# Optimization experiments

Measured on AMD Instinct MI355X. Metric: run time of the kernel, lower is better.

Reference implementation:

```python
import jax, jax.numpy as jnp
import numpy as np

B, T, D = 1, 2048, 4096
H, G = 32, 8
HD = D // H          # 128
REP = H // G         # 4
KV_DIM = 2 * HD * G  # 2048


def setup_inputs() -> dict:
    key = jax.random.key(0)
    k0, k1, k2, k3 = jax.random.split(key, 4)
    x = jax.random.normal(k0, (B, T, D), dtype=jnp.float32)
    Wq = jax.random.normal(k1, (D, D), dtype=jnp.float32) * 0.02
    Wkv = jax.random.normal(k2, (D, KV_DIM), dtype=jnp.float32) * 0.02
    Wo = jax.random.normal(k3, (D, D), dtype=jnp.float32) * 0.02
    bo = jnp.zeros((D,), dtype=jnp.float32)
    return {"x": x, "Wq": Wq, "Wkv": Wkv, "Wo": Wo, "bo": bo}


def reference(x, Wq, Wkv, Wo, bo):
    b, t, d = x.shape
    # projections (qkv_bias=False)
    q = jnp.dot(x, Wq).reshape(b, t, H, HD).transpose(0, 2, 1, 3)        # (b,H,t,hd)
    kv = jnp.dot(x, Wkv).reshape(b, t, G, 2, HD).transpose(2, 3, 0, 1, 4)  # (G,2,b,t,hd)
    k, v = kv[:, 0], kv[:, 1]                                             # (G,b,t,hd)
    # faithful to torch: unsqueeze+repeat then flat view(b, H, t, hd)
    k = jnp.broadcast_to(k[:, :, None], (G, b, REP, t, HD)).reshape(b, H, t, HD)
    v = jnp.broadcast_to(v[:, :, None], (G, b, REP, t, HD)).reshape(b, H, t, HD)
    # attention: mask then scale, matching original order
    scores = jnp.einsum('bhqd,bhkd->bhqk', q, k)                          # (b,H,t,t)
    causal = jnp.triu(jnp.ones((t, t), dtype=bool), 1)
    scores = jnp.where(causal[None, None], -jnp.inf, scores)
    weights = jax.nn.softmax(scores * (1.0 / HD ** 0.5), axis=-1)
    ctx = jnp.einsum('bhqk,bhkd->bhqd', weights, v)                       # (b,H,t,hd)
    ctx = ctx.transpose(0, 2, 1, 3).reshape(b, t, d)
    return jnp.dot(ctx, Wo) + bo
```

## Files before the change

kernel.cpp:

```cpp
#include <hip/hip_runtime.h>

#define T_SEQ 2048
#define D_MODEL 4096
#define NH 32
#define NG 8
#define HD 128

typedef unsigned short u16;
typedef __bf16 bf16x8 __attribute__((ext_vector_type(8)));
typedef float f32x4 __attribute__((ext_vector_type(4)));

#define AS1 __attribute__((address_space(1)))
#define AS3 __attribute__((address_space(3)))

__device__ __forceinline__ void async_cp16(const u16* g, u16* l) {
  __builtin_amdgcn_global_load_lds((AS1 void*)g, (AS3 void*)l, 16, 0, 0);
}

__device__ __forceinline__ u16 f2bf(float f){
  union { float f; unsigned x; } v; v.f = f;
  unsigned r = v.x + 0x7FFFu + ((v.x >> 16) & 1u);
  return (u16)(r >> 16);
}
__device__ __forceinline__ u16 to_bf(float f){ return f2bf(f); }
__device__ __forceinline__ u16 to_bf(u16 u){ return u; }

__global__ __launch_bounds__(256) void cvt_k(const float* __restrict__ in,
                                             u16* __restrict__ out, int n4)
{
  int i = blockIdx.x * 256 + threadIdx.x;
  if (i >= n4) return;
  float4 v = *(const float4*)&in[(size_t)i * 4];
  short4 o;
  o.x = (short)f2bf(v.x); o.y = (short)f2bf(v.y);
  o.z = (short)f2bf(v.z); o.w = (short)f2bf(v.w);
  *(short4*)&out[(size_t)i * 4] = o;
}

template<typename TIN>
__global__ __launch_bounds__(256) void transpose_k(const TIN* __restrict__ in,
                                                   u16* __restrict__ out, int R, int C)
{
  __shared__ __align__(16) u16 tile[32][36];
  int c0 = blockIdx.x * 32, r0 = blockIdx.y * 32;
  int t = threadIdx.x;
  int lr = t >> 3, lc = (t & 7) * 4;
  const TIN* src = &in[(size_t)(r0 + lr) * C + c0 + lc];
  #pragma unroll
  for (int i = 0; i < 4; i++) tile[lr][lc + i] = to_bf(src[i]);
  __syncthreads();
  short4 v;
  v.x = (short)tile[lc + 0][lr];
  v.y = (short)tile[lc + 1][lr];
  v.z = (short)tile[lc + 2][lr];
  v.w = (short)tile[lc + 3][lr];
  *(short4*)&out[(size_t)(c0 + lr) * R + r0 + lc] = v;
}

template<int MODE>
__global__ __launch_bounds__(256) void gemm_k(
    const u16* __restrict__ A, const u16* __restrict__ BT,
    u16* __restrict__ Cout, u16* __restrict__ Kout, u16* __restrict__ Vout,
    float* __restrict__ Fout, const float* __restrict__ bias, int K, int N)
{
  __shared__ __align__(16) u16 sA[2 * 128 * 64];
  __shared__ __align__(16) u16 sB[2 * 128 * 64];
  const int t = threadIdx.x;
  const int lane = t & 63, wave = t >> 6;
  const int quad = lane >> 4, lm = lane & 15;
  const int wm = wave >> 1, wn = wave & 1;
  const int m0 = blockIdx.y * 128, n0 = blockIdx.x * 128;
  const int ntk = K >> 6;
  const f32x4 fzero = {0.f, 0.f, 0.f, 0.f};

  const int sr_sub = lane >> 3;
  const int sgl = (lane & 7) ^ sr_sub;

  f32x4 acc[4][4];
  #pragma unroll
  for (int i = 0; i < 4; i++)
    #pragma unroll
    for (int j = 0; j < 4; j++) acc[i][j] = fzero;

  auto stage = [&](int td) {
    const int k0 = td << 6;
    u16* dA = sA + (td & 1) * (128 * 64);
    u16* dB = sB + (td & 1) * (128 * 64);
    #pragma unroll
    for (int c = 0; c < 4; c++) {
      int r = c * 32 + wave * 8 + sr_sub;
      async_cp16(&A [(size_t)(m0 + r) * K + k0 + sgl * 8], &dA[(c * 256 + wave * 64) * 8]);
      async_cp16(&BT[(size_t)(n0 + r) * K + k0 + sgl * 8], &dB[(c * 256 + wave * 64) * 8]);
    }
  };

  stage(0);
  stage(1);

  for (int ti = 0; ti < ntk; ++ti) {
    if (ti + 1 < ntk) { asm volatile("s_waitcnt vmcnt(8)" ::: "memory"); }
    else             { asm volatile("s_waitcnt vmcnt(0)" ::: "memory"); }
    __builtin_amdgcn_s_barrier();
    asm volatile("" ::: "memory");

    const u16* cA = sA + (ti & 1) * (128 * 64);
    const u16* cB = sB + (ti & 1) * (128 * 64);

    __builtin_amdgcn_s_setprio(1);
    #pragma unroll
    for (int kb = 0; kb < 2; kb++) {
      bf16x8 af[4], bfr[4];
      #pragma unroll
      for (int mt = 0; mt < 4; mt++) {
        int row = wm * 64 + mt * 16 + lm;
        af[mt] = *(const bf16x8*)&cA[row * 64 + (((kb * 4 + quad) ^ (lm & 7)) * 8)];
      }
      #pragma unroll
      for (int nt = 0; nt < 4; nt++) {
        int row = wn * 64 + nt * 16 + lm;
        bfr[nt] = *(const bf16x8*)&cB[row * 64 + (((kb * 4 + quad) ^ (lm & 7)) * 8)];
      }
      #pragma unroll
      for (int mt = 0; mt < 4; mt++)
        #pragma unroll
        for (int nt = 0; nt < 4; nt++)
          acc[mt][nt] = __builtin_amdgcn_mfma_f32_16x16x32_bf16(af[mt], bfr[nt], acc[mt][nt], 0, 0, 0);
    }
    __builtin_amdgcn_s_setprio(0);

    __builtin_amdgcn_s_barrier();
    asm volatile("" ::: "memory");
    if (ti + 2 < ntk) stage(ti + 2);
  }

  #pragma unroll
  for (int mt = 0; mt < 4; mt++) {
    #pragma unroll
    for (int nt = 0; nt < 4; nt++) {
      int gcol = n0 + wn * 64 + nt * 16 + lm;
      int grow0 = m0 + wm * 64 + mt * 16 + quad * 4;
      if (MODE == 1) {
        if (gcol < 4096) {
          #pragma unroll
          for (int r = 0; r < 4; r++)
            Cout[(size_t)(grow0 + r) * 4096 + gcol] = f2bf(acc[mt][nt][r]);
        } else {
          int c = gcol - 4096;
          int g = c >> 8, s = (c >> 7) & 1, hd = c & 127;
          if (s) {
            short4 pv;
            pv.x = (short)f2bf(acc[mt][nt][0]);
            pv.y = (short)f2bf(acc[mt][nt][1]);
            pv.z = (short)f2bf(acc[mt][nt][2]);
            pv.w = (short)f2bf(acc[mt][nt][3]);
            *(short4*)&Vout[((size_t)g * HD + hd) * T_SEQ + grow0] = pv;
          } else {
            #pragma unroll
            for (int r = 0; r < 4; r++)
              Kout[((size_t)g * T_SEQ + grow0 + r) * HD + hd] = f2bf(acc[mt][nt][r]);
          }
        }
      } else {
        #pragma unroll
        for (int r = 0; r < 4; r++)
          Fout[(size_t)(grow0 + r) * N + gcol] = acc[mt][nt][r] + bias[gcol];
      }
    }
  }
}

__global__ __launch_bounds__(256) void attn_k(
    const u16* __restrict__ Q, const u16* __restrict__ Kb,
    const u16* __restrict__ Vt, u16* __restrict__ ctx)
{
  __shared__ __align__(16) u16 sK[2 * 64 * 128];
  __shared__ __align__(16) u16 sV[2 * 128 * 64];
  __shared__ __align__(16) u16 sP[4 * 16 * 72];
  const int t = threadIdx.x;
  const int lane = t & 63, wave = t >> 6;
  const int quad = lane >> 4, lm = lane & 15;

  const int id = blockIdx.x + gridDim.x * blockIdx.y;
  const int g = id & 7;
  const int idx = id >> 3;
  const int h = g * 4 + (idx & 3);
  const int q0 = (31 - (idx >> 2)) * 64;
  const int nt = (q0 >> 6) + 1;

  const float scale = 0.088388347648318447f;
  const float C1 = scale * 1.4426950408889634f;
  const float C2 = -14.0f * 1.4426950408889634f;
  const f32x4 fzero = {0.f, 0.f, 0.f, 0.f};

  bf16x8 aq[4];
  {
    const u16* qp = Q + (size_t)(q0 + wave * 16 + lm) * D_MODEL + h * HD + quad * 8;
    #pragma unroll
    for (int kb = 0; kb < 4; kb++) aq[kb] = *(const bf16x8*)(qp + kb * 32);
  }
  bf16x8 bones;
  #pragma unroll
  for (int i = 0; i < 8; i++) bones[i] = (__bf16)1.0f;

  f32x4 o[8];
  #pragma unroll
  for (int i = 0; i < 8; i++) o[i] = fzero;
  f32x4 lacc = fzero;

  const u16* Kg = Kb + (size_t)g * T_SEQ * HD;
  const u16* Vg = Vt + (size_t)g * HD * T_SEQ;
  u16* sPw = sP + wave * 16 * 72;

  const int k_r_sub = lane >> 4;
  const int v_r_sub = lane >> 3;
  const int v_gl = (lane & 7) ^ v_r_sub;

  auto stage = [&](int td) {
    const int kv0 = td << 6;
    u16* dK = sK + (td & 1) * (64 * 128);
    u16* dV = sV + (td & 1) * (128 * 64);
    #pragma unroll
    for (int c = 0; c < 4; c++) {
      int rk = c * 16 + wave * 4 + k_r_sub;
      int kgl = (lane & 15) ^ (rk & 7);
      async_cp16(&Kg[(size_t)(kv0 + rk) * HD + kgl * 8], &dK[(c * 256 + wave * 64) * 8]);
      int rv = c * 32 + wave * 8 + v_r_sub;
      async_cp16(&Vg[(size_t)rv * T_SEQ + kv0 + v_gl * 8], &dV[(c * 256 + wave * 64) * 8]);
    }
  };

  stage(0);
  if (nt > 1) stage(1);

  for (int ti = 0; ti < nt; ++ti) {
    if (ti + 1 < nt) { asm volatile("s_waitcnt vmcnt(8)" ::: "memory"); }
    else             { asm volatile("s_waitcnt vmcnt(0)" ::: "memory"); }
    __builtin_amdgcn_s_barrier();
    asm volatile("" ::: "memory");

    const u16* cK = sK + (ti & 1) * (64 * 128);
    const u16* cV = sV + (ti & 1) * (128 * 64);
    const int kv0 = ti << 6;

    f32x4 s[4];
    __builtin_amdgcn_s_setprio(1);
    #pragma unroll
    for (int nt4 = 0; nt4 < 4; nt4++) {
      s[nt4] = fzero;
      #pragma unroll
      for (int kb = 0; kb < 4; kb++) {
        int row = nt4 * 16 + lm;
        bf16x8 bk = *(const bf16x8*)&cK[row * 128 + (((kb * 4 + quad) ^ (lm & 7)) * 8)];
        s[nt4] = __builtin_amdgcn_mfma_f32_16x16x32_bf16(aq[kb], bk, s[nt4], 0, 0, 0);
      }
    }
    __builtin_amdgcn_s_setprio(0);

    if (ti == nt - 1) {
      #pragma unroll
      for (int r = 0; r < 4; r++) {
        int qr = q0 + wave * 16 + quad * 4 + r;
        #pragma unroll
        for (int nt4 = 0; nt4 < 4; nt4++) {
          int kvc = kv0 + nt4 * 16 + lm;
          float p = exp2f(fmaf(s[nt4][r], C1, C2));
          p = (kvc > qr) ? 0.f : p;
          sPw[(quad * 4 + r) * 72 + nt4 * 16 + lm] = f2bf(p);
        }
      }
    } else {
      #pragma unroll
      for (int r = 0; r < 4; r++) {
        #pragma unroll
        for (int nt4 = 0; nt4 < 4; nt4++) {
          float p = exp2f(fmaf(s[nt4][r], C1, C2));
          sPw[(quad * 4 + r) * 72 + nt4 * 16 + lm] = f2bf(p);
        }
      }
    }

    __builtin_amdgcn_s_setprio(1);
    #pragma unroll
    for (int kb2 = 0; kb2 < 2; kb2++) {
      bf16x8 ap = *(const bf16x8*)&sPw[lm * 72 + kb2 * 32 + quad * 8];
      lacc = __builtin_amdgcn_mfma_f32_16x16x32_bf16(ap, bones, lacc, 0, 0, 0);
      #pragma unroll
      for (int n8 = 0; n8 < 8; n8++) {
        int row = n8 * 16 + lm;
        bf16x8 bv = *(const bf16x8*)&cV[row * 64 + (((kb2 * 4 + quad) ^ (lm & 7)) * 8)];
        o[n8] = __builtin_amdgcn_mfma_f32_16x16x32_bf16(ap, bv, o[n8], 0, 0, 0);
      }
    }
    __builtin_amdgcn_s_setprio(0);

    __builtin_amdgcn_s_barrier();
    asm volatile("" ::: "memory");
    if (ti + 2 < nt) stage(ti + 2);
  }

  #pragma unroll
  for (int r = 0; r < 4; r++) {
    float inv = 1.f / lacc[r];
    #pragma unroll
    for (int n8 = 0; n8 < 8; n8++) {
      ctx[(size_t)(q0 + wave * 16 + quad * 4 + r) * D_MODEL + h * HD + n8 * 16 + lm]
          = f2bf(o[n8][r] * inv);
    }
  }
}

extern "C" void kernel_launch(void* const* d_in, const int* in_sizes, int n_in,
                              void* d_out, int out_size, void* d_ws, size_t ws_size,
                              hipStream_t stream)
{
  const float* x   = (const float*)d_in[0];
  const float* Wq  = (const float*)d_in[1];
  const float* Wkv = (const float*)d_in[2];
  const float* Wo  = (const float*)d_in[3];
  const float* bo  = (const float*)d_in[4];
  float* out = (float*)d_out;

  char* ws = (char*)d_ws;
  const size_t SZ_T   = 50331648;
  const size_t SZ_ACT = 16777216;
  const size_t SZ_KV  = 4194304;
  u16* Tb = (u16*)(ws);
  u16* Xb = (u16*)(ws + SZ_T);
  u16* Qb = (u16*)(ws + SZ_T + SZ_ACT);
  u16* Kb = (u16*)(ws + SZ_T + 2 * SZ_ACT);
  u16* Vt = (u16*)(ws + SZ_T + 2 * SZ_ACT + SZ_KV);
  u16* Cx = Xb;

  cvt_k<<<dim3(8192, 1, 1), 256, 0, stream>>>(x, Xb, 2097152);
  transpose_k<float><<<dim3(128, 128, 1), 256, 0, stream>>>(Wq, Tb, 4096, 4096);
  transpose_k<float><<<dim3(64, 128, 1), 256, 0, stream>>>(Wkv, Tb + (size_t)4096 * 4096, 4096, 2048);
  gemm_k<1><<<dim3(48, 16, 1), 256, 0, stream>>>(Xb, Tb, Qb, Kb, Vt, nullptr, nullptr, 4096, 6144);
  attn_k<<<dim3(32, 32, 1), 256, 0, stream>>>(Qb, Kb, Vt, Cx);
  transpose_k<float><<<dim3(128, 128, 1), 256, 0, stream>>>(Wo, Tb, 4096, 4096);
  gemm_k<2><<<dim3(32, 16, 1), 256, 0, stream>>>(Cx, Tb, nullptr, nullptr, nullptr, out, bo, 4096, 4096);
}
```

Before: 473.2 us.

## Halve GEMM K-tile to 32 with new LDS swizzle for higher occupancy

The GEMM K-step drops from 64 to 32, which halves the LDS footprint per block. The async copy mapping and XOR swizzle are reworked for 32-wide rows, and launch bounds now request 5 blocks per CU to raise occupancy. The transpose kernel also switches to vectorized float4/short4 loads. In exchange there are twice as many barrier and wait iterations per GEMM, with less MFMA work between them to hide latency.

```diff
diff --git a/kernel.cpp b/kernel.cpp
--- a/kernel.cpp
+++ b/kernel.cpp
@@ -22,8 +22,6 @@
   unsigned r = v.x + 0x7FFFu + ((v.x >> 16) & 1u);
   return (u16)(r >> 16);
 }
-__device__ __forceinline__ u16 to_bf(float f){ return f2bf(f); }
-__device__ __forceinline__ u16 to_bf(u16 u){ return u; }
 
 __global__ __launch_bounds__(256) void cvt_k(const float* __restrict__ in,
                                              u16* __restrict__ out, int n4)
@@ -46,8 +44,19 @@
   int t = threadIdx.x;
   int lr = t >> 3, lc = (t & 7) * 4;
   const TIN* src = &in[(size_t)(r0 + lr) * C + c0 + lc];
-  #pragma unroll
-  for (int i = 0; i < 4; i++) tile[lr][lc + i] = to_bf(src[i]);
+  if constexpr (sizeof(TIN) == 4) {
+    float4 v4 = *(const float4*)src;
+    tile[lr][lc + 0] = f2bf(v4.x);
+    tile[lr][lc + 1] = f2bf(v4.y);
+    tile[lr][lc + 2] = f2bf(v4.z);
+    tile[lr][lc + 3] = f2bf(v4.w);
+  } else {
+    short4 v4 = *(const short4*)src;
+    tile[lr][lc + 0] = (u16)v4.x;
+    tile[lr][lc + 1] = (u16)v4.y;
+    tile[lr][lc + 2] = (u16)v4.z;
+    tile[lr][lc + 3] = (u16)v4.w;
+  }
   __syncthreads();
   short4 v;
   v.x = (short)tile[lc + 0][lr];
@@ -58,23 +67,25 @@
 }
 
 template<int MODE>
-__global__ __launch_bounds__(256) void gemm_k(
+__global__ __launch_bounds__(256, 5) void gemm_k(
     const u16* __restrict__ A, const u16* __restrict__ BT,
     u16* __restrict__ Cout, u16* __restrict__ Kout, u16* __restrict__ Vout,
     float* __restrict__ Fout, const float* __restrict__ bias, int K, int N)
 {
-  __shared__ __align__(16) u16 sA[2 * 128 * 64];
-  __shared__ __align__(16) u16 sB[2 * 128 * 64];
+  __shared__ __align__(16) u16 sA[2 * 128 * 32];
+  __shared__ __align__(16) u16 sB[2 * 128 * 32];
   const int t = threadIdx.x;
   const int lane = t & 63, wave = t >> 6;
   const int quad = lane >> 4, lm = lane & 15;
   const int wm = wave >> 1, wn = wave & 1;
   const int m0 = blockIdx.y * 128, n0 = blockIdx.x * 128;
-  const int ntk = K >> 6;
+  const int ntk = K >> 5;
   const f32x4 fzero = {0.f, 0.f, 0.f, 0.f};
 
-  const int sr_sub = lane >> 3;
-  const int sgl = (lane & 7) ^ sr_sub;
+  const int sr = lane >> 2;
+  const int sg = lane & 3;
+  const int sgl = sg ^ ((sr >> 1) & 3);
+  const int rphys = (quad ^ ((lm >> 1) & 3)) * 8;
 
   f32x4 acc[4][4];
   #pragma unroll
@@ -83,14 +94,14 @@
     for (int j = 0; j < 4; j++) acc[i][j] = fzero;
 
   auto stage = [&](int td) {
-    const int k0 = td << 6;
-    u16* dA = sA + (td & 1) * (128 * 64);
-    u16* dB = sB + (td & 1) * (128 * 64);
-    #pragma unroll
-    for (int c = 0; c < 4; c++) {
-      int r = c * 32 + wave * 8 + sr_sub;
-      async_cp16(&A [(size_t)(m0 + r) * K + k0 + sgl * 8], &dA[(c * 256 + wave * 64) * 8]);
-      async_cp16(&BT[(size_t)(n0 + r) * K + k0 + sgl * 8], &dB[(c * 256 + wave * 64) * 8]);
+    const int k0 = td << 5;
+    u16* dA = sA + (td & 1) * (128 * 32);
+    u16* dB = sB + (td & 1) * (128 * 32);
+    #pragma unroll
+    for (int c = 0; c < 2; c++) {
+      int r = c * 64 + wave * 16 + sr;
+      async_cp16(&A [(size_t)(m0 + r) * K + k0 + sgl * 8], &dA[(c * 64 + wave * 16) * 32]);
+      async_cp16(&BT[(size_t)(n0 + r) * K + k0 + sgl * 8], &dB[(c * 64 + wave * 16) * 32]);
     }
   };
 
@@ -98,34 +109,27 @@
   stage(1);
 
   for (int ti = 0; ti < ntk; ++ti) {
-    if (ti + 1 < ntk) { asm volatile("s_waitcnt vmcnt(8)" ::: "memory"); }
+    if (ti + 1 < ntk) { asm volatile("s_waitcnt vmcnt(4)" ::: "memory"); }
     else             { asm volatile("s_waitcnt vmcnt(0)" ::: "memory"); }
     __builtin_amdgcn_s_barrier();
     asm volatile("" ::: "memory");
 
-    const u16* cA = sA + (ti & 1) * (128 * 64);
-    const u16* cB = sB + (ti & 1) * (128 * 64);
+    const u16* cA = sA + (ti & 1) * (128 * 32);
+    const u16* cB = sB + (ti & 1) * (128 * 32);
 
     __builtin_amdgcn_s_setprio(1);
-    #pragma unroll
-    for (int kb = 0; kb < 2; kb++) {
-      bf16x8 af[4], bfr[4];
-      #pragma unroll
-      for (int mt = 0; mt < 4; mt++) {
-        int row = wm * 64 + mt * 16 + lm;
-        af[mt] = *(const bf16x8*)&cA[row * 64 + (((kb * 4 + quad) ^ (lm & 7)) * 8)];
-      }
-      #pragma unroll
-      for (int nt = 0; nt < 4; nt++) {
-        int row = wn * 64 + nt * 16 + lm;
-        bfr[nt] = *(const bf16x8*)&cB[row * 64 + (((kb * 4 + quad) ^ (lm & 7)) * 8)];
-      }
-      #pragma unroll
-      for (int mt = 0; mt < 4; mt++)
-        #pragma unroll
-        for (int nt = 0; nt < 4; nt++)
-          acc[mt][nt] = __builtin_amdgcn_mfma_f32_16x16x32_bf16(af[mt], bfr[nt], acc[mt][nt], 0, 0, 0);
-    }
+    bf16x8 af[4], bfr[4];
+    #pragma unroll
+    for (int mt = 0; mt < 4; mt++)
+      af[mt] = *(const bf16x8*)&cA[(wm * 64 + mt * 16 + lm) * 32 + rphys];
+    #pragma unroll
+    for (int nt = 0; nt < 4; nt++)
+      bfr[nt] = *(const bf16x8*)&cB[(wn * 64 + nt * 16 + lm) * 32 + rphys];
+    #pragma unroll
+    for (int mt = 0; mt < 4; mt++)
+      #pragma unroll
+      for (int nt = 0; nt < 4; nt++)
+        acc[mt][nt] = __builtin_amdgcn_mfma_f32_16x16x32_bf16(af[mt], bfr[nt], acc[mt][nt], 0, 0, 0);
     __builtin_amdgcn_s_setprio(0);
 
     __builtin_amdgcn_s_barrier();
```

Measured after the change: 554.8 us. 17.2% more time.
